# Optimization experiments

Hardware: AMD Instinct MI355X
Metric: run time of the kernel (lower is better)

The kernel has to match this reference:

```python
import jax, jax.numpy as jnp
import numpy as np

EPS = 1e-8  # torch CosineSimilarity eps
TEMP = 0.05

def _l2norm(x):
    n = jnp.sqrt(jnp.sum(x * x, axis=-1, keepdims=True))
    return x / jnp.maximum(n, EPS)

def setup_inputs() -> dict:
    key = jax.random.key(0)
    k1, k2, k3 = jax.random.split(key, 3)
    query = jax.random.normal(k1, (256, 768), dtype=jnp.float32)
    keys = jax.random.normal(k2, (256, 768), dtype=jnp.float32)
    queue = jax.random.normal(k3, (64, 1024, 768), dtype=jnp.float32)
    return {"query": query, "keys": keys, "queue": queue}

def reference(query, keys, queue):
    B, D = query.shape
    qn = _l2norm(query)                       # [B, D]
    kn = _l2norm(keys)                        # [B, D]
    negn = _l2norm(queue.reshape(-1, D))      # [N, D]
    sim_pos = jnp.einsum('bd,cd->bc', qn, kn)   # [B, B]
    sim_neg = jnp.einsum('bd,nd->bn', qn, negn) # [B, N]
    logits = jnp.concatenate([sim_pos, sim_neg], axis=1) / TEMP  # [B, B+N]
    target = jnp.arange(B)
    logp = jax.nn.log_softmax(logits, axis=-1)
    loss = -jnp.mean(logp[jnp.arange(B), target])
    return loss
```

## Files before the change

### kernel.cpp

```cpp
#include <hip/hip_runtime.h>
#include <hip/hip_bf16.h>

typedef __attribute__((ext_vector_type(8))) short short8;
typedef __attribute__((ext_vector_type(4))) float f32x4;

#define TEMP_INV 20.0f
#define NCH 256

__device__ inline unsigned short f2bf(float f){
    unsigned int u = __builtin_bit_cast(unsigned int, f);
    u += 0x7fffu + ((u >> 16) & 1u);
    return (unsigned short)(u >> 16);
}
__device__ inline float bf2f(unsigned short h){
    unsigned int u = ((unsigned int)h) << 16;
    return __builtin_bit_cast(float, u);
}
__device__ inline unsigned int pk2bf(float a, float b){
    return (unsigned int)f2bf(a) | ((unsigned int)f2bf(b) << 16);
}

#define GLOAD16(src, dst) __builtin_amdgcn_global_load_lds( \
    (const __attribute__((address_space(1))) unsigned int*)(src), \
    (__attribute__((address_space(3))) unsigned int*)(dst), 16, 0, 0)

__global__ __launch_bounds__(256) void k_norm(const float* __restrict__ q,
                                              unsigned short* __restrict__ Aswz){
    int b = blockIdx.x, t = threadIdx.x;
    const float* qr = q + b * 768;
    float v0 = qr[t], v1 = qr[t + 256], v2 = qr[t + 512];
    float ss = v0*v0 + v1*v1 + v2*v2;
#pragma unroll
    for (int o = 32; o; o >>= 1) ss += __shfl_xor(ss, o);
    __shared__ float red[4];
    if ((t & 63) == 0) red[t >> 6] = ss;
    __syncthreads();
    ss = red[0] + red[1] + red[2] + red[3];
    float inv = 1.0f / fmaxf(sqrtf(ss), 1e-8f);
    float nv[3] = {v0 * inv, v1 * inv, v2 * inv};
#pragma unroll
    for (int j = 0; j < 3; j++){
        int cc = t + 256 * j;
        unsigned short h = f2bf(nv[j]);
        int kc = cc >> 6, kl = cc & 63, g = kl >> 3, e = kl & 7;
        int slot = g ^ (b & 7);
        Aswz[kc * 16384 + b * 64 + slot * 8 + e] = h;
    }
}

__global__ __launch_bounds__(1024, 1) void k_main(
        const float* __restrict__ keys,
        const float* __restrict__ queue,
        const unsigned short* __restrict__ Aswz,
        float* __restrict__ pmax,
        float* __restrict__ psum,
        float* __restrict__ diag){
    __shared__ unsigned short Atile[2][16384];
    __shared__ unsigned short Btile[8192];
    __shared__ float bxnf[768];
    __shared__ unsigned short bxn16[768];
    __shared__ float invn[128];
    __shared__ float redm[4][256];
    __shared__ float reds[4][256];
    __shared__ float xred[4][256];
    __shared__ float wred[16];
    __shared__ float sxs;

    const int b = blockIdx.x, t = threadIdx.x;
    const int lane = t & 63;
    const int w = t >> 6;
    const int wm = w >> 2, wn = w & 3;
    const int frow = lane & 15, fg = lane >> 4;
    const int c = t >> 3, q8 = t & 7;

    size_t rx = (size_t)b * 257;
    float ssx = 0.f;
    if (t < 768){ float v = queue[rx * 768 + t]; bxnf[t] = v; ssx = v * v; }
#pragma unroll
    for (int o = 32; o; o >>= 1) ssx += __shfl_xor(ssx, o);
    if (lane == 0) wred[w] = ssx;
    __syncthreads();
    if (t == 0){
        float s = 0.f;
#pragma unroll
        for (int i = 0; i < 16; i++) s += wred[i];
        sxs = 1.0f / fmaxf(sqrtf(s), 1e-8f);
    }
    __syncthreads();
    if (t < 768) bxn16[t] = f2bf(bxnf[t] * sxs);
    __syncthreads();

    long n0 = (long)b * 257 + c;
    long n1 = n0 + 128;
    const float* rp0 = ((n0 < 256) ? (keys + n0 * 768)
                                   : (queue + (size_t)(n0 - 256) * 768)) + q8 * 4;
    const float* rp1 = ((n1 < 256) ? (keys + n1 * 768)
                                   : (queue + (size_t)(n1 - 256) * 768)) + q8 * 4;

    {
        const unsigned short* gA = Aswz + t * 8;
        GLOAD16(gA, &Atile[0][t * 8]);
        GLOAD16(gA + 8192, &Atile[0][t * 8 + 8192]);
    }
    float4 cb0 = *(const float4*)(rp0);
    float4 cb1 = *(const float4*)(rp0 + 32);

    float Mrun = -1e30f, Srun = 0.f;
    float dx = 0.f;
    const int xrow = t & 255, xk = t >> 8;

    for (int p = 0; p < 2; ++p){
        const float* rp = p ? rp1 : rp0;
        float ssq = 0.f;
        f32x4 acc[4][2];
#pragma unroll
        for (int i = 0; i < 4; i++)
#pragma unroll
            for (int j = 0; j < 2; j++) acc[i][j] = (f32x4)0.f;

        for (int kc = 0; kc < 12; ++kc){
            const int s = p * 12 + kc;
            const bool lastStep = (s == 23);
            float4 nb0 = cb0, nb1 = cb1;
            if (!lastStep){
                const int sn = s + 1;
                const int kcn = (kc < 11) ? (kc + 1) : 0;
                const unsigned short* gA = Aswz + kcn * 16384 + t * 8;
                unsigned short* lA = &Atile[sn & 1][t * 8];
                GLOAD16(gA, lA);
                GLOAD16(gA + 8192, lA + 8192);
                const float* rpn = (kc < 11) ? rp : rp1;
                nb0 = *(const float4*)(rpn + kcn * 64);
                nb1 = *(const float4*)(rpn + kcn * 64 + 32);
                asm volatile("s_waitcnt vmcnt(4)" ::: "memory");
            } else {
                asm volatile("s_waitcnt vmcnt(0)" ::: "memory");
            }

            {
                float4 u = cb0;
                ssq += u.x*u.x + u.y*u.y + u.z*u.z + u.w*u.w;
                int idx = q8;
                int slot = (idx >> 1) ^ (c & 7);
                uint2 pk;
                pk.x = pk2bf(u.x, u.y);
                pk.y = pk2bf(u.z, u.w);
                *(uint2*)&Btile[c * 64 + slot * 8 + (idx & 1) * 4] = pk;
                u = cb1;
                ssq += u.x*u.x + u.y*u.y + u.z*u.z + u.w*u.w;
                idx = q8 + 8;
                slot = (idx >> 1) ^ (c & 7);
                pk.x = pk2bf(u.x, u.y);
                pk.y = pk2bf(u.z, u.w);
                *(uint2*)&Btile[c * 64 + slot * 8 + (idx & 1) * 4] = pk;
            }
            asm volatile("s_waitcnt lgkmcnt(0)" ::: "memory");
            __builtin_amdgcn_s_barrier();
            asm volatile("" ::: "memory");

#pragma unroll
            for (int ks = 0; ks < 2; ++ks){
                short8 af[4], bfv[2];
#pragma unroll
                for (int fm = 0; fm < 4; ++fm){
                    int row = wm * 64 + fm * 16 + frow;
                    int slot = (ks * 4 + fg) ^ (frow & 7);
                    af[fm] = *(const short8*)&Atile[s & 1][row * 64 + slot * 8];
                }
#pragma unroll
                for (int fn = 0; fn < 2; ++fn){
                    int row = wn * 32 + fn * 16 + frow;
                    int slot = (ks * 4 + fg) ^ (frow & 7);
                    bfv[fn] = *(const short8*)&Btile[row * 64 + slot * 8];
                }
#pragma unroll
                for (int fm = 0; fm < 4; ++fm)
#pragma unroll
                    for (int fn = 0; fn < 2; ++fn)
                        acc[fm][fn] = __builtin_amdgcn_mfma_f32_16x16x32_bf16(
                            af[fm], bfv[fn], acc[fm][fn], 0, 0, 0);
            }

            if (p == 0){
#pragma unroll
                for (int gi = 0; gi < 2; ++gi){
                    int g = xk * 2 + gi;
                    short8 av = *(const short8*)&Atile[kc & 1][xrow * 64 + (g ^ (xrow & 7)) * 8];
                    short8 xv = *(const short8*)&bxn16[kc * 64 + g * 8];
#pragma unroll
                    for (int e = 0; e < 8; ++e)
                        dx += bf2f((unsigned short)av[e]) * bf2f((unsigned short)xv[e]);
                }
            }

            __builtin_amdgcn_s_barrier();
            asm volatile("" ::: "memory");
            cb0 = nb0; cb1 = nb1;
        }

        ssq += __shfl_xor(ssq, 1);
        ssq += __shfl_xor(ssq, 2);
        ssq += __shfl_xor(ssq, 4);
        if (q8 == 0) invn[c] = 1.0f / fmaxf(sqrtf(ssq), 1e-8f);
        if (p == 0) xred[xk][xrow] = dx;
        __syncthreads();

#pragma unroll
        for (int fm = 0; fm < 4; ++fm){
#pragma unroll
            for (int rr = 0; rr < 4; ++rr){
                float v0 = acc[fm][0][rr] * invn[wn * 32 + frow] * TEMP_INV;
                float v1 = acc[fm][1][rr] * invn[wn * 32 + 16 + frow] * TEMP_INV;
                int row = wm * 64 + fm * 16 + fg * 4 + rr;
                if (b == 0){
                    int col0 = p * 128 + wn * 32 + frow;
                    if (row == col0)      diag[row] = v0;
                    if (row == col0 + 16) diag[row] = v1;
                }
                float m = fmaxf(v0, v1);
#pragma unroll
                for (int o = 1; o < 16; o <<= 1) m = fmaxf(m, __shfl_xor(m, o));
                float s = __expf(v0 - m) + __expf(v1 - m);
#pragma unroll
                for (int o = 1; o < 16; o <<= 1) s += __shfl_xor(s, o);
                if (frow == 0){ redm[wn][row] = m; reds[wn][row] = s; }
            }
        }
        __syncthreads();
        if (t < 256){
#pragma unroll
            for (int ww = 0; ww < 4; ++ww){
                float m2 = redm[ww][t], s2 = reds[ww][t];
                float M = fmaxf(Mrun, m2);
                Srun = Srun * __expf(Mrun - M) + s2 * __expf(m2 - M);
                Mrun = M;
            }
        }
        __syncthreads();
    }

    if (t < 256){
        float vx = (xred[0][t] + xred[1][t] + xred[2][t] + xred[3][t]) * TEMP_INV;
        float M = fmaxf(Mrun, vx);
        float S = Srun * __expf(Mrun - M) + __expf(vx - M);
        pmax[b * 256 + t] = M;
        psum[b * 256 + t] = S;
    }
}

__global__ __launch_bounds__(256) void k_lse(const float* __restrict__ pmax,
                                             const float* __restrict__ psum,
                                             const float* __restrict__ diag,
                                             float* __restrict__ lossb){
    int b = blockIdx.x, t = threadIdx.x;
    float m = -1e30f;
    for (int cc = t; cc < NCH; cc += 256) m = fmaxf(m, pmax[cc * 256 + b]);
#pragma unroll
    for (int o = 32; o; o >>= 1) m = fmaxf(m, __shfl_xor(m, o));
    __shared__ float red[4];
    __shared__ float Msh;
    if ((t & 63) == 0) red[t >> 6] = m;
    __syncthreads();
    if (t == 0) Msh = fmaxf(fmaxf(red[0], red[1]), fmaxf(red[2], red[3]));
    __syncthreads();
    float M = Msh;
    float s = 0.f;
    for (int cc = t; cc < NCH; cc += 256) s += psum[cc * 256 + b] * __expf(pmax[cc * 256 + b] - M);
#pragma unroll
    for (int o = 32; o; o >>= 1) s += __shfl_xor(s, o);
    if ((t & 63) == 0) red[t >> 6] = s;
    __syncthreads();
    if (t == 0) lossb[b] = M + logf(red[0] + red[1] + red[2] + red[3]) - diag[b];
}

__global__ __launch_bounds__(256) void k_red(const float* __restrict__ lossb,
                                             float* __restrict__ out){
    int t = threadIdx.x;
    float v = lossb[t];
#pragma unroll
    for (int o = 32; o; o >>= 1) v += __shfl_xor(v, o);
    __shared__ float red[4];
    if ((t & 63) == 0) red[t >> 6] = v;
    __syncthreads();
    if (t == 0) out[0] = (red[0] + red[1] + red[2] + red[3]) * (1.0f / 256.0f);
}

extern "C" void kernel_launch(void* const* d_in, const int* in_sizes, int n_in,
                              void* d_out, int out_size, void* d_ws, size_t ws_size,
                              hipStream_t stream){
    const float* q  = (const float*)d_in[0];
    const float* k  = (const float*)d_in[1];
    const float* qu = (const float*)d_in[2];
    char* ws = (char*)d_ws;
    unsigned short* Aswz = (unsigned short*)(ws);
    float* diag  = (float*)(ws + 393216);
    float* pmax  = (float*)(ws + 394240);
    float* psum  = (float*)(ws + 656384);
    float* lossb = (float*)(ws + 918528);

    k_norm<<<256, 256, 0, stream>>>(q, Aswz);
    k_main<<<256, 1024, 0, stream>>>(k, qu, Aswz, pmax, psum, diag);
    k_lse<<<256, 256, 0, stream>>>(pmax, psum, diag, lossb);
    k_red<<<1, 256, 0, stream>>>(lossb, (float*)d_out);
}
```

Measured before the change: 71.24 us.

## Double-buffer B tile, flatten k-loop, and fuse final reduction via atomicAdd

Double-buffers the B tile in LDS and prefetches B rows two steps ahead, so staging the next B chunk overlaps the current MFMA step and one barrier per iteration goes away. The two passes are flattened into a single 24-step loop, with the first pass's softmax epilogue placed at step 11. The separate final reduction kernel is removed: k_lse atomically adds each row's scaled loss into the output, which k_norm now zeroes. This saves a kernel launch and some barrier stalls, at the cost of extra LDS and a float atomic sum whose ordering is nondeterministic.

```diff
diff --git a/kernel.cpp b/kernel.cpp
--- a/kernel.cpp
+++ b/kernel.cpp
@@ -25,8 +25,10 @@
     (__attribute__((address_space(3))) unsigned int*)(dst), 16, 0, 0)
 
 __global__ __launch_bounds__(256) void k_norm(const float* __restrict__ q,
-                                              unsigned short* __restrict__ Aswz){
+                                              unsigned short* __restrict__ Aswz,
+                                              float* __restrict__ out){
     int b = blockIdx.x, t = threadIdx.x;
+    if (b == 0 && t == 0) out[0] = 0.f;
     const float* qr = q + b * 768;
     float v0 = qr[t], v1 = qr[t + 256], v2 = qr[t + 512];
     float ss = v0*v0 + v1*v1 + v2*v2;
@@ -56,7 +58,7 @@
         float* __restrict__ psum,
         float* __restrict__ diag){
     __shared__ unsigned short Atile[2][16384];
-    __shared__ unsigned short Btile[8192];
+    __shared__ unsigned short Btile[2][8192];
     __shared__ float bxnf[768];
     __shared__ unsigned short bxn16[768];
     __shared__ float invn[128];
@@ -72,6 +74,7 @@
     const int wm = w >> 2, wn = w & 3;
     const int frow = lane & 15, fg = lane >> 4;
     const int c = t >> 3, q8 = t & 7;
+    const int c7 = c & 7;
 
     size_t rx = (size_t)b * 257;
     float ssx = 0.f;
@@ -97,114 +100,168 @@
     const float* rp1 = ((n1 < 256) ? (keys + n1 * 768)
                                    : (queue + (size_t)(n1 - 256) * 768)) + q8 * 4;
 
+    float ssqA = 0.f, ssqB = 0.f;
+
+    auto stageB = [&](unsigned short* bt, float4 u0, float4 u1, float& sq){
+        sq += u0.x*u0.x + u0.y*u0.y + u0.z*u0.z + u0.w*u0.w;
+        sq += u1.x*u1.x + u1.y*u1.y + u1.z*u1.z + u1.w*u1.w;
+        int slot0 = (q8 >> 1) ^ c7;
+        int slot1 = ((q8 + 8) >> 1) ^ c7;
+        uint2 pk0, pk1;
+        pk0.x = pk2bf(u0.x, u0.y); pk0.y = pk2bf(u0.z, u0.w);
+        pk1.x = pk2bf(u1.x, u1.y); pk1.y = pk2bf(u1.z, u1.w);
+        *(uint2*)&bt[c * 64 + slot0 * 8 + (q8 & 1) * 4] = pk0;
+        *(uint2*)&bt[c * 64 + slot1 * 8 + (q8 & 1) * 4] = pk1;
+    };
+
     {
         const unsigned short* gA = Aswz + t * 8;
         GLOAD16(gA, &Atile[0][t * 8]);
         GLOAD16(gA + 8192, &Atile[0][t * 8 + 8192]);
     }
-    float4 cb0 = *(const float4*)(rp0);
-    float4 cb1 = *(const float4*)(rp0 + 32);
+    float4 cur0 = *(const float4*)(rp0);
+    float4 cur1 = *(const float4*)(rp0 + 32);
+    float4 nxt0 = *(const float4*)(rp0 + 64);
+    float4 nxt1 = *(const float4*)(rp0 + 96);
+    asm volatile("s_waitcnt vmcnt(2)" ::: "memory");
+    stageB(Btile[0], cur0, cur1, ssqA);
+    asm volatile("s_waitcnt lgkmcnt(0)" ::: "memory");
+    __builtin_amdgcn_s_barrier();
+    asm volatile("" ::: "memory");
+    cur0 = nxt0; cur1 = nxt1;
 
     float Mrun = -1e30f, Srun = 0.f;
     float dx = 0.f;
     const int xrow = t & 255, xk = t >> 8;
 
-    for (int p = 0; p < 2; ++p){
-        const float* rp = p ? rp1 : rp0;
-        float ssq = 0.f;
-        f32x4 acc[4][2];
-#pragma unroll
-        for (int i = 0; i < 4; i++)
-#pragma unroll
-            for (int j = 0; j < 2; j++) acc[i][j] = (f32x4)0.f;
-
-        for (int kc = 0; kc < 12; ++kc){
-            const int s = p * 12 + kc;
-            const bool lastStep = (s == 23);
-            float4 nb0 = cb0, nb1 = cb1;
-            if (!lastStep){
-                const int sn = s + 1;
-                const int kcn = (kc < 11) ? (kc + 1) : 0;
-                const unsigned short* gA = Aswz + kcn * 16384 + t * 8;
-                unsigned short* lA = &Atile[sn & 1][t * 8];
-                GLOAD16(gA, lA);
-                GLOAD16(gA + 8192, lA + 8192);
-                const float* rpn = (kc < 11) ? rp : rp1;
-                nb0 = *(const float4*)(rpn + kcn * 64);
-                nb1 = *(const float4*)(rpn + kcn * 64 + 32);
-                asm volatile("s_waitcnt vmcnt(4)" ::: "memory");
-            } else {
-                asm volatile("s_waitcnt vmcnt(0)" ::: "memory");
-            }
-
-            {
-                float4 u = cb0;
-                ssq += u.x*u.x + u.y*u.y + u.z*u.z + u.w*u.w;
-                int idx = q8;
-                int slot = (idx >> 1) ^ (c & 7);
-                uint2 pk;
-                pk.x = pk2bf(u.x, u.y);
-                pk.y = pk2bf(u.z, u.w);
-                *(uint2*)&Btile[c * 64 + slot * 8 + (idx & 1) * 4] = pk;
-                u = cb1;
-                ssq += u.x*u.x + u.y*u.y + u.z*u.z + u.w*u.w;
-                idx = q8 + 8;
-                slot = (idx >> 1) ^ (c & 7);
-                pk.x = pk2bf(u.x, u.y);
-                pk.y = pk2bf(u.z, u.w);
-                *(uint2*)&Btile[c * 64 + slot * 8 + (idx & 1) * 4] = pk;
-            }
-            asm volatile("s_waitcnt lgkmcnt(0)" ::: "memory");
-            __builtin_amdgcn_s_barrier();
-            asm volatile("" ::: "memory");
-
-#pragma unroll
-            for (int ks = 0; ks < 2; ++ks){
-                short8 af[4], bfv[2];
-#pragma unroll
-                for (int fm = 0; fm < 4; ++fm){
-                    int row = wm * 64 + fm * 16 + frow;
-                    int slot = (ks * 4 + fg) ^ (frow & 7);
-                    af[fm] = *(const short8*)&Atile[s & 1][row * 64 + slot * 8];
+    f32x4 acc[4][2];
+#pragma unroll
+    for (int i = 0; i < 4; i++)
+#pragma unroll
+        for (int j = 0; j < 2; j++) acc[i][j] = (f32x4)0.f;
+
+    for (int s = 0; s < 24; ++s){
+        if (s < 23){
+            int kcn = (s + 1) % 12;
+            const unsigned short* gA = Aswz + kcn * 16384 + t * 8;
+            unsigned short* lA = &Atile[(s + 1) & 1][t * 8];
+            GLOAD16(gA, lA);
+            GLOAD16(gA + 8192, lA + 8192);
+        }
+        float4 nb0 = cur0, nb1 = cur1;
+        if (s < 22){
+            int u = s + 2;
+            const float* rpu = (u < 12) ? rp0 : rp1;
+            int kcu = (u < 12) ? u : (u - 12);
+            nb0 = *(const float4*)(rpu + kcu * 64);
+            nb1 = *(const float4*)(rpu + kcu * 64 + 32);
+        }
+        if (s < 22)       asm volatile("s_waitcnt vmcnt(4)" ::: "memory");
+        else if (s == 22) asm volatile("s_waitcnt vmcnt(2)" ::: "memory");
+        else              asm volatile("s_waitcnt vmcnt(0)" ::: "memory");
+
+        if (s < 23){
+            int u = s + 1;
+            if (u < 12) stageB(Btile[(s + 1) & 1], cur0, cur1, ssqA);
+            else        stageB(Btile[(s + 1) & 1], cur0, cur1, ssqB);
+        }
+
+        const unsigned short* At = Atile[s & 1];
+        const unsigned short* Bt = Btile[s & 1];
+#pragma unroll
+        for (int ks = 0; ks < 2; ++ks){
+            short8 af[4], bfv[2];
+#pragma unroll
+            for (int fm = 0; fm < 4; ++fm){
+                int row = wm * 64 + fm * 16 + frow;
+                int slot = (ks * 4 + fg) ^ (frow & 7);
+                af[fm] = *(const short8*)&At[row * 64 + slot * 8];
+            }
+#pragma unroll
+            for (int fn = 0; fn < 2; ++fn){
+                int row = wn * 32 + fn * 16 + frow;
+                int slot = (ks * 4 + fg) ^ (frow & 7);
+                bfv[fn] = *(const short8*)&Bt[row * 64 + slot * 8];
+            }
+#pragma unroll
+            for (int fm = 0; fm < 4; ++fm)
+#pragma unroll
+                for (int fn = 0; fn < 2; ++fn)
+                    acc[fm][fn] = __builtin_amdgcn_mfma_f32_16x16x32_bf16(
+                        af[fm], bfv[fn], acc[fm][fn], 0, 0, 0);
+        }
+
+        if (s < 12){
+#pragma unroll
+            for (int gi = 0; gi < 2; ++gi){
+                int g = xk * 2 + gi;
+                short8 av = *(const short8*)&At[xrow * 64 + (g ^ (xrow & 7)) * 8];
+                short8 xv = *(const short8*)&bxn16[s * 64 + g * 8];
+#pragma unroll
+                for (int e = 0; e < 8; ++e)
+                    dx += bf2f((unsigned short)av[e]) * bf2f((unsigned short)xv[e]);
+            }
+        }
+
+        asm volatile("s_waitcnt lgkmcnt(0)" ::: "memory");
+        __builtin_amdgcn_s_barrier();
+        asm volatile("" ::: "memory");
+        cur0 = nb0; cur1 = nb1;
+
+        if (s == 11){
+            float sq = ssqA;
+            sq += __shfl_xor(sq, 1);
+            sq += __shfl_xor(sq, 2);
+            sq += __shfl_xor(sq, 4);
+            if (q8 == 0) invn[c] = 1.0f / fmaxf(sqrtf(sq), 1e-8f);
+            xred[xk][xrow] = dx;
+            __syncthreads();
+#pragma unroll
+            for (int fm = 0; fm < 4; ++fm){
+#pragma unroll
+                for (int rr = 0; rr < 4; ++rr){
+                    float v0 = acc[fm][0][rr] * invn[wn * 32 + frow] * TEMP_INV;
+                    float v1 = acc[fm][1][rr] * invn[wn * 32 + 16 + frow] * TEMP_INV;
+                    int row = wm * 64 + fm * 16 + fg * 4 + rr;
+                    if (b == 0){
+                        int col0 = wn * 32 + frow;
+                        if (row == col0)      diag[row] = v0;
+                        if (row == col0 + 16) diag[row] = v1;
+                    }
+                    float m = fmaxf(v0, v1);
+#pragma unroll
+                    for (int o = 1; o < 16; o <<= 1) m = fmaxf(m, __shfl_xor(m, o));
+                    float sex = __expf(v0 - m) + __expf(v1 - m);
+#pragma unroll
+                    for (int o = 1; o < 16; o <<= 1) sex += __shfl_xor(sex, o);
+                    if (frow == 0){ redm[wn][row] = m; reds[wn][row] = sex; }
                 }
-#pragma unroll
-                for (int fn = 0; fn < 2; ++fn){
-                    int row = wn * 32 + fn * 16 + frow;
-                    int slot = (ks * 4 + fg) ^ (frow & 7);
-                    bfv[fn] = *(const short8*)&Btile[row * 64 + slot * 8];
+            }
+            __syncthreads();
+            if (t < 256){
+#pragma unroll
+                for (int ww = 0; ww < 4; ++ww){
+                    float m2 = redm[ww][t], s2 = reds[ww][t];
+                    float M = fmaxf(Mrun, m2);
+                    Srun = Srun * __expf(Mrun - M) + s2 * __expf(m2 - M);
+                    Mrun = M;
                 }
-#pragma unroll
-                for (int fm = 0; fm < 4; ++fm)
-#pragma unroll
-                    for (int fn = 0; fn < 2; ++fn)
-                        acc[fm][fn] = __builtin_amdgcn_mfma_f32_16x16x32_bf16(
-                            af[fm], bfv[fn], acc[fm][fn], 0, 0, 0);
-            }
-
-            if (p == 0){
-#pragma unroll
-                for (int gi = 0; gi < 2; ++gi){
-                    int g = xk * 2 + gi;
-                    short8 av = *(const short8*)&Atile[kc & 1][xrow * 64 + (g ^ (xrow & 7)) * 8];
-                    short8 xv = *(const short8*)&bxn16[kc * 64 + g * 8];
-#pragma unroll
-                    for (int e = 0; e < 8; ++e)
-                        dx += bf2f((unsigned short)av[e]) * bf2f((unsigned short)xv[e]);
-                }
-            }
-
-            __builtin_amdgcn_s_barrier();
-            asm volatile("" ::: "memory");
-            cb0 = nb0; cb1 = nb1;
-        }
-
-        ssq += __shfl_xor(ssq, 1);
-        ssq += __shfl_xor(ssq, 2);
-        ssq += __shfl_xor(ssq, 4);
-        if (q8 == 0) invn[c] = 1.0f / fmaxf(sqrtf(ssq), 1e-8f);
-        if (p == 0) xred[xk][xrow] = dx;
+            }
+            __syncthreads();
+#pragma unroll
+            for (int i = 0; i < 4; i++)
+#pragma unroll
+                for (int j = 0; j < 2; j++) acc[i][j] = (f32x4)0.f;
+        }
+    }
+
+    {
+        float sq = ssqB;
+        sq += __shfl_xor(sq, 1);
+        sq += __shfl_xor(sq, 2);
+        sq += __shfl_xor(sq, 4);
+        if (q8 == 0) invn[c] = 1.0f / fmaxf(sqrtf(sq), 1e-8f);
         __syncthreads();
-
 #pragma unroll
         for (int fm = 0; fm < 4; ++fm){
 #pragma unroll
@@ -213,17 +270,17 @@
                 float v1 = acc[fm][1][rr] * invn[wn * 32 + 16 + frow] * TEMP_INV;
                 int row = wm * 64 + fm * 16 + fg * 4 + rr;
                 if (b == 0){
-                    int col0 = p * 128 + wn * 32 + frow;
+                    int col0 = 128 + wn * 32 + frow;
                     if (row == col0)      diag[row] = v0;
                     if (row == col0 + 16) diag[row] = v1;
                 }
                 float m = fmaxf(v0, v1);
 #pragma unroll
                 for (int o = 1; o < 16; o <<= 1) m = fmaxf(m, __shfl_xor(m, o));
-                float s = __expf(v0 - m) + __expf(v1 - m);
-#pragma unroll
-                for (int o = 1; o < 16; o <<= 1) s += __shfl_xor(s, o);
-                if (frow == 0){ redm[wn][row] = m; reds[wn][row] = s; }
+                float sex = __expf(v0 - m) + __expf(v1 - m);
+#pragma unroll
+                for (int o = 1; o < 16; o <<= 1) sex += __shfl_xor(sex, o);
+                if (frow == 0){ redm[wn][row] = m; reds[wn][row] = sex; }
             }
         }
         __syncthreads();
@@ -236,7 +293,6 @@
                 Mrun = M;
             }
         }
-        __syncthreads();
     }
 
     if (t < 256){
@@ -251,7 +307,7 @@
 __global__ __launch_bounds__(256) void k_lse(const float* __restrict__ pmax,
                                              const float* __restrict__ psum,
                                              const float* __restrict__ diag,
-                                             float* __restrict__ lossb){
+                                             float* __restrict__ out){
     int b = blockIdx.x, t = threadIdx.x;
     float m = -1e30f;
     for (int cc = t; cc < NCH; cc += 256) m = fmaxf(m, pmax[cc * 256 + b]);
@@ -270,19 +326,8 @@
     for (int o = 32; o; o >>= 1) s += __shfl_xor(s, o);
     if ((t & 63) == 0) red[t >> 6] = s;
     __syncthreads();
-    if (t == 0) lossb[b] = M + logf(red[0] + red[1] + red[2] + red[3]) - diag[b];
-}
-
-__global__ __launch_bounds__(256) void k_red(const float* __restrict__ lossb,
-                                             float* __restrict__ out){
-    int t = threadIdx.x;
-    float v = lossb[t];
-#pragma unroll
-    for (int o = 32; o; o >>= 1) v += __shfl_xor(v, o);
-    __shared__ float red[4];
-    if ((t & 63) == 0) red[t >> 6] = v;
-    __syncthreads();
-    if (t == 0) out[0] = (red[0] + red[1] + red[2] + red[3]) * (1.0f / 256.0f);
+    if (t == 0)
+        atomicAdd(out, (M + logf(red[0] + red[1] + red[2] + red[3]) - diag[b]) * (1.0f / 256.0f));
 }
 
 extern "C" void kernel_launch(void* const* d_in, const int* in_sizes, int n_in,
@@ -296,10 +341,8 @@
     float* diag  = (float*)(ws + 393216);
     float* pmax  = (float*)(ws + 394240);
     float* psum  = (float*)(ws + 656384);
-    float* lossb = (float*)(ws + 918528);
-
-    k_norm<<<256, 256, 0, stream>>>(q, Aswz);
+
+    k_norm<<<256, 256, 0, stream>>>(q, Aswz, (float*)d_out);
     k_main<<<256, 1024, 0, stream>>>(k, qu, Aswz, pmax, psum, diag);
-    k_lse<<<256, 256, 0, stream>>>(pmax, psum, diag, lossb);
-    k_red<<<1, 256, 0, stream>>>(lossb, (float*)d_out);
-}
+    k_lse<<<256, 256, 0, stream>>>(pmax, psum, diag, (float*)d_out);
+}
```

Measured after the change: 71.31 us. Within noise of the previous version (+0.1%).

## Split main GEMM into 1024 smaller blocks and fuse final reduction via atomics

Applied to the files above, without the earlier changes.

The main kernel now runs 1024 blocks of 512 threads, each handling 64 queue rows, instead of 256 blocks of 1024 threads handling 257 rows. Keys are handled only as a single-row diagonal dot product in the first 256 blocks, since only the diagonal of the positive block is used. The explicit double-buffered A prefetch with manual waitcnt is replaced by a simple load-sync-compute loop that relies on multiple resident blocks per CU for latency hiding. The final reduction kernel is dropped in favour of an atomicAdd into the zeroed output, which introduces a nondeterministic summation order.

```diff
diff --git a/kernel.cpp b/kernel.cpp
--- a/kernel.cpp
+++ b/kernel.cpp
@@ -5,7 +5,7 @@
 typedef __attribute__((ext_vector_type(4))) float f32x4;
 
 #define TEMP_INV 20.0f
-#define NCH 256
+#define NCH 1024
 
 __device__ inline unsigned short f2bf(float f){
     unsigned int u = __builtin_bit_cast(unsigned int, f);
@@ -25,8 +25,10 @@
     (__attribute__((address_space(3))) unsigned int*)(dst), 16, 0, 0)
 
 __global__ __launch_bounds__(256) void k_norm(const float* __restrict__ q,
-                                              unsigned short* __restrict__ Aswz){
+                                              unsigned short* __restrict__ Aswz,
+                                              float* __restrict__ out){
     int b = blockIdx.x, t = threadIdx.x;
+    if (b == 0 && t == 0) out[0] = 0.f;
     const float* qr = q + b * 768;
     float v0 = qr[t], v1 = qr[t + 256], v2 = qr[t + 512];
     float ss = v0*v0 + v1*v1 + v2*v2;
@@ -48,201 +50,154 @@
     }
 }
 
-__global__ __launch_bounds__(1024, 1) void k_main(
+__global__ __launch_bounds__(512, 4) void k_main(
         const float* __restrict__ keys,
         const float* __restrict__ queue,
         const unsigned short* __restrict__ Aswz,
         float* __restrict__ pmax,
         float* __restrict__ psum,
         float* __restrict__ diag){
-    __shared__ unsigned short Atile[2][16384];
-    __shared__ unsigned short Btile[8192];
-    __shared__ float bxnf[768];
+    __shared__ unsigned short Atile[16384];
+    __shared__ unsigned short Btile[4096];
     __shared__ unsigned short bxn16[768];
-    __shared__ float invn[128];
-    __shared__ float redm[4][256];
-    __shared__ float reds[4][256];
-    __shared__ float xred[4][256];
-    __shared__ float wred[16];
+    __shared__ float invn[64];
+    __shared__ float redm[2][256];
+    __shared__ float reds[2][256];
+    __shared__ float xred[2][256];
+    __shared__ float wred[8];
     __shared__ float sxs;
 
     const int b = blockIdx.x, t = threadIdx.x;
     const int lane = t & 63;
     const int w = t >> 6;
-    const int wm = w >> 2, wn = w & 3;
+    const int wm = w >> 1, wn = w & 1;
     const int frow = lane & 15, fg = lane >> 4;
-    const int c = t >> 3, q8 = t & 7;
-
-    size_t rx = (size_t)b * 257;
-    float ssx = 0.f;
-    if (t < 768){ float v = queue[rx * 768 + t]; bxnf[t] = v; ssx = v * v; }
-#pragma unroll
-    for (int o = 32; o; o >>= 1) ssx += __shfl_xor(ssx, o);
-    if (lane == 0) wred[w] = ssx;
-    __syncthreads();
-    if (t == 0){
-        float s = 0.f;
-#pragma unroll
-        for (int i = 0; i < 16; i++) s += wred[i];
-        sxs = 1.0f / fmaxf(sqrtf(s), 1e-8f);
-    }
-    __syncthreads();
-    if (t < 768) bxn16[t] = f2bf(bxnf[t] * sxs);
-    __syncthreads();
-
-    long n0 = (long)b * 257 + c;
-    long n1 = n0 + 128;
-    const float* rp0 = ((n0 < 256) ? (keys + n0 * 768)
-                                   : (queue + (size_t)(n0 - 256) * 768)) + q8 * 4;
-    const float* rp1 = ((n1 < 256) ? (keys + n1 * 768)
-                                   : (queue + (size_t)(n1 - 256) * 768)) + q8 * 4;
-
-    {
-        const unsigned short* gA = Aswz + t * 8;
-        GLOAD16(gA, &Atile[0][t * 8]);
-        GLOAD16(gA + 8192, &Atile[0][t * 8 + 8192]);
-    }
-    float4 cb0 = *(const float4*)(rp0);
-    float4 cb1 = *(const float4*)(rp0 + 32);
-
-    float Mrun = -1e30f, Srun = 0.f;
-    float dx = 0.f;
+    const int r = t >> 3, q8 = t & 7;
+    const bool keyblk = (b < 256);
+
+    if (keyblk){
+        const float* krow = keys + b * 768;
+        float v0 = krow[t];
+        float v1 = (t < 256) ? krow[512 + t] : 0.f;
+        float ssx = v0 * v0 + v1 * v1;
+#pragma unroll
+        for (int o = 32; o; o >>= 1) ssx += __shfl_xor(ssx, o);
+        if (lane == 0) wred[w] = ssx;
+        __syncthreads();
+        if (t == 0){
+            float s = 0.f;
+#pragma unroll
+            for (int i = 0; i < 8; i++) s += wred[i];
+            sxs = 1.0f / fmaxf(sqrtf(s), 1e-8f);
+        }
+        __syncthreads();
+        bxn16[t] = f2bf(v0 * sxs);
+        if (t < 256) bxn16[512 + t] = f2bf(v1 * sxs);
+        __syncthreads();
+    }
+
+    const float* rp = queue + (size_t)(b * 64 + r) * 768 + q8 * 4;
     const int xrow = t & 255, xk = t >> 8;
 
-    for (int p = 0; p < 2; ++p){
-        const float* rp = p ? rp1 : rp0;
-        float ssq = 0.f;
-        f32x4 acc[4][2];
+    float ssq = 0.f, dx = 0.f;
+    f32x4 acc[4][2];
+#pragma unroll
+    for (int i = 0; i < 4; i++)
+#pragma unroll
+        for (int j = 0; j < 2; j++) acc[i][j] = (f32x4)0.f;
+
+    for (int kc = 0; kc < 12; ++kc){
+        if (kc) __syncthreads();
 #pragma unroll
         for (int i = 0; i < 4; i++)
-#pragma unroll
-            for (int j = 0; j < 2; j++) acc[i][j] = (f32x4)0.f;
-
-        for (int kc = 0; kc < 12; ++kc){
-            const int s = p * 12 + kc;
-            const bool lastStep = (s == 23);
-            float4 nb0 = cb0, nb1 = cb1;
-            if (!lastStep){
-                const int sn = s + 1;
-                const int kcn = (kc < 11) ? (kc + 1) : 0;
-                const unsigned short* gA = Aswz + kcn * 16384 + t * 8;
-                unsigned short* lA = &Atile[sn & 1][t * 8];
-                GLOAD16(gA, lA);
-                GLOAD16(gA + 8192, lA + 8192);
-                const float* rpn = (kc < 11) ? rp : rp1;
-                nb0 = *(const float4*)(rpn + kcn * 64);
-                nb1 = *(const float4*)(rpn + kcn * 64 + 32);
-                asm volatile("s_waitcnt vmcnt(4)" ::: "memory");
-            } else {
-                asm volatile("s_waitcnt vmcnt(0)" ::: "memory");
+            GLOAD16(Aswz + kc * 16384 + i * 4096 + t * 8,
+                    Atile + i * 4096 + t * 8);
+        float4 u0 = *(const float4*)(rp + kc * 64);
+        float4 u1 = *(const float4*)(rp + kc * 64 + 32);
+        ssq += u0.x*u0.x + u0.y*u0.y + u0.z*u0.z + u0.w*u0.w;
+        ssq += u1.x*u1.x + u1.y*u1.y + u1.z*u1.z + u1.w*u1.w;
+        {
+            int slot0 = (q8 >> 1) ^ (r & 7);
+            int slot1 = ((q8 + 8) >> 1) ^ (r & 7);
+            uint2 pk0, pk1;
+            pk0.x = pk2bf(u0.x, u0.y); pk0.y = pk2bf(u0.z, u0.w);
+            pk1.x = pk2bf(u1.x, u1.y); pk1.y = pk2bf(u1.z, u1.w);
+            *(uint2*)&Btile[r * 64 + slot0 * 8 + (q8 & 1) * 4] = pk0;
+            *(uint2*)&Btile[r * 64 + slot1 * 8 + (q8 & 1) * 4] = pk1;
+        }
+        __syncthreads();
+
+#pragma unroll
+        for (int ks = 0; ks < 2; ++ks){
+            short8 af[4], bfv[2];
+#pragma unroll
+            for (int fm = 0; fm < 4; ++fm){
+                int row = wm * 64 + fm * 16 + frow;
+                int slot = (ks * 4 + fg) ^ (frow & 7);
+                af[fm] = *(const short8*)&Atile[row * 64 + slot * 8];
             }
-
-            {
-                float4 u = cb0;
-                ssq += u.x*u.x + u.y*u.y + u.z*u.z + u.w*u.w;
-                int idx = q8;
-                int slot = (idx >> 1) ^ (c & 7);
-                uint2 pk;
-                pk.x = pk2bf(u.x, u.y);
-                pk.y = pk2bf(u.z, u.w);
-                *(uint2*)&Btile[c * 64 + slot * 8 + (idx & 1) * 4] = pk;
-                u = cb1;
-                ssq += u.x*u.x + u.y*u.y + u.z*u.z + u.w*u.w;
-                idx = q8 + 8;
-                slot = (idx >> 1) ^ (c & 7);
-                pk.x = pk2bf(u.x, u.y);
-                pk.y = pk2bf(u.z, u.w);
-                *(uint2*)&Btile[c * 64 + slot * 8 + (idx & 1) * 4] = pk;
+#pragma unroll
+            for (int fn = 0; fn < 2; ++fn){
+                int row = wn * 32 + fn * 16 + frow;
+                int slot = (ks * 4 + fg) ^ (frow & 7);
+                bfv[fn] = *(const short8*)&Btile[row * 64 + slot * 8];
             }
-            asm volatile("s_waitcnt lgkmcnt(0)" ::: "memory");
-            __builtin_amdgcn_s_barrier();
-            asm volatile("" ::: "memory");
-
-#pragma unroll
-            for (int ks = 0; ks < 2; ++ks){
-                short8 af[4], bfv[2];
-#pragma unroll
-                for (int fm = 0; fm < 4; ++fm){
-                    int row = wm * 64 + fm * 16 + frow;
-                    int slot = (ks * 4 + fg) ^ (frow & 7);
-                    af[fm] = *(const short8*)&Atile[s & 1][row * 64 + slot * 8];
-                }
-#pragma unroll
-                for (int fn = 0; fn < 2; ++fn){
-                    int row = wn * 32 + fn * 16 + frow;
-                    int slot = (ks * 4 + fg) ^ (frow & 7);
-                    bfv[fn] = *(const short8*)&Btile[row * 64 + slot * 8];
-                }
-#pragma unroll
-                for (int fm = 0; fm < 4; ++fm)
-#pragma unroll
-                    for (int fn = 0; fn < 2; ++fn)
-                        acc[fm][fn] = __builtin_amdgcn_mfma_f32_16x16x32_bf16(
-                            af[fm], bfv[fn], acc[fm][fn], 0, 0, 0);
+#pragma unroll
+            for (int fm = 0; fm < 4; ++fm)
+#pragma unroll
+                for (int fn = 0; fn < 2; ++fn)
+                    acc[fm][fn] = __builtin_amdgcn_mfma_f32_16x16x32_bf16(
+                        af[fm], bfv[fn], acc[fm][fn], 0, 0, 0);
+        }
+
+        if (keyblk){
+#pragma unroll
+            for (int gi = 0; gi < 4; ++gi){
+                int g = xk * 4 + gi;
+                short8 av = *(const short8*)&Atile[xrow * 64 + (g ^ (xrow & 7)) * 8];
+                short8 xv = *(const short8*)&bxn16[kc * 64 + g * 8];
+#pragma unroll
+                for (int e = 0; e < 8; ++e)
+                    dx += bf2f((unsigned short)av[e]) * bf2f((unsigned short)xv[e]);
             }
-
-            if (p == 0){
-#pragma unroll
-                for (int gi = 0; gi < 2; ++gi){
-                    int g = xk * 2 + gi;
-                    short8 av = *(const short8*)&Atile[kc & 1][xrow * 64 + (g ^ (xrow & 7)) * 8];
-                    short8 xv = *(const short8*)&bxn16[kc * 64 + g * 8];
-#pragma unroll
-                    for (int e = 0; e < 8; ++e)
-                        dx += bf2f((unsigned short)av[e]) * bf2f((unsigned short)xv[e]);
-                }
-            }
-
-            __builtin_amdgcn_s_barrier();
-            asm volatile("" ::: "memory");
-            cb0 = nb0; cb1 = nb1;
-        }
-
-        ssq += __shfl_xor(ssq, 1);
-        ssq += __shfl_xor(ssq, 2);
-        ssq += __shfl_xor(ssq, 4);
-        if (q8 == 0) invn[c] = 1.0f / fmaxf(sqrtf(ssq), 1e-8f);
-        if (p == 0) xred[xk][xrow] = dx;
-        __syncthreads();
-
-#pragma unroll
-        for (int fm = 0; fm < 4; ++fm){
-#pragma unroll
-            for (int rr = 0; rr < 4; ++rr){
-                float v0 = acc[fm][0][rr] * invn[wn * 32 + frow] * TEMP_INV;
-                float v1 = acc[fm][1][rr] * invn[wn * 32 + 16 + frow] * TEMP_INV;
-                int row = wm * 64 + fm * 16 + fg * 4 + rr;
-                if (b == 0){
-                    int col0 = p * 128 + wn * 32 + frow;
-                    if (row == col0)      diag[row] = v0;
-                    if (row == col0 + 16) diag[row] = v1;
-                }
-                float m = fmaxf(v0, v1);
-#pragma unroll
-                for (int o = 1; o < 16; o <<= 1) m = fmaxf(m, __shfl_xor(m, o));
-                float s = __expf(v0 - m) + __expf(v1 - m);
-#pragma unroll
-                for (int o = 1; o < 16; o <<= 1) s += __shfl_xor(s, o);
-                if (frow == 0){ redm[wn][row] = m; reds[wn][row] = s; }
-            }
-        }
-        __syncthreads();
-        if (t < 256){
-#pragma unroll
-            for (int ww = 0; ww < 4; ++ww){
-                float m2 = redm[ww][t], s2 = reds[ww][t];
-                float M = fmaxf(Mrun, m2);
-                Srun = Srun * __expf(Mrun - M) + s2 * __expf(m2 - M);
-                Mrun = M;
-            }
-        }
-        __syncthreads();
-    }
-
+        }
+    }
+
+    ssq += __shfl_xor(ssq, 1);
+    ssq += __shfl_xor(ssq, 2);
+    ssq += __shfl_xor(ssq, 4);
+    if (q8 == 0) invn[r] = 1.0f / fmaxf(sqrtf(ssq), 1e-8f);
+    if (keyblk) xred[xk][xrow] = dx;
+    __syncthreads();
+
+#pragma unroll
+    for (int fm = 0; fm < 4; ++fm){
+#pragma unroll
+        for (int rr = 0; rr < 4; ++rr){
+            float v0 = acc[fm][0][rr] * invn[wn * 32 + frow] * TEMP_INV;
+            float v1 = acc[fm][1][rr] * invn[wn * 32 + 16 + frow] * TEMP_INV;
+            int row = wm * 64 + fm * 16 + fg * 4 + rr;
+            float m = fmaxf(v0, v1);
+#pragma unroll
+            for (int o = 1; o < 16; o <<= 1) m = fmaxf(m, __shfl_xor(m, o));
+            float s = __expf(v0 - m) + __expf(v1 - m);
+#pragma unroll
+            for (int o = 1; o < 16; o <<= 1) s += __shfl_xor(s, o);
+            if (frow == 0){ redm[wn][row] = m; reds[wn][row] = s; }
+        }
+    }
+    __syncthreads();
     if (t < 256){
-        float vx = (xred[0][t] + xred[1][t] + xred[2][t] + xred[3][t]) * TEMP_INV;
-        float M = fmaxf(Mrun, vx);
-        float S = Srun * __expf(Mrun - M) + __expf(vx - M);
+        float m0 = redm[0][t], m1 = redm[1][t];
+        float M = fmaxf(m0, m1);
+        float S = reds[0][t] * __expf(m0 - M) + reds[1][t] * __expf(m1 - M);
+        if (keyblk){
+            float vx = (xred[0][t] + xred[1][t]) * TEMP_INV;
+            if (t == b) diag[b] = vx;
+            float M2 = fmaxf(M, vx);
+            S = S * __expf(M - M2) + __expf(vx - M2);
+            M = M2;
+        }
         pmax[b * 256 + t] = M;
         psum[b * 256 + t] = S;
     }
@@ -251,7 +206,7 @@
 __global__ __launch_bounds__(256) void k_lse(const float* __restrict__ pmax,
                                              const float* __restrict__ psum,
                                              const float* __restrict__ diag,
-                                             float* __restrict__ lossb){
+                                             float* __restrict__ out){
     int b = blockIdx.x, t = threadIdx.x;
     float m = -1e30f;
     for (int cc = t; cc < NCH; cc += 256) m = fmaxf(m, pmax[cc * 256 + b]);
@@ -270,19 +225,8 @@
     for (int o = 32; o; o >>= 1) s += __shfl_xor(s, o);
     if ((t & 63) == 0) red[t >> 6] = s;
     __syncthreads();
-    if (t == 0) lossb[b] = M + logf(red[0] + red[1] + red[2] + red[3]) - diag[b];
-}
-
-__global__ __launch_bounds__(256) void k_red(const float* __restrict__ lossb,
-                                             float* __restrict__ out){
-    int t = threadIdx.x;
-    float v = lossb[t];
-#pragma unroll
-    for (int o = 32; o; o >>= 1) v += __shfl_xor(v, o);
-    __shared__ float red[4];
-    if ((t & 63) == 0) red[t >> 6] = v;
-    __syncthreads();
-    if (t == 0) out[0] = (red[0] + red[1] + red[2] + red[3]) * (1.0f / 256.0f);
+    if (t == 0)
+        atomicAdd(out, (M + logf(red[0] + red[1] + red[2] + red[3]) - diag[b]) * (1.0f / 256.0f));
 }
 
 extern "C" void kernel_launch(void* const* d_in, const int* in_sizes, int n_in,
@@ -295,11 +239,9 @@
     unsigned short* Aswz = (unsigned short*)(ws);
     float* diag  = (float*)(ws + 393216);
     float* pmax  = (float*)(ws + 394240);
-    float* psum  = (float*)(ws + 656384);
-    float* lossb = (float*)(ws + 918528);
-
-    k_norm<<<256, 256, 0, stream>>>(q, Aswz);
-    k_main<<<256, 1024, 0, stream>>>(k, qu, Aswz, pmax, psum, diag);
-    k_lse<<<256, 256, 0, stream>>>(pmax, psum, diag, lossb);
-    k_red<<<1, 256, 0, stream>>>(lossb, (float*)d_out);
-}
+    float* psum  = (float*)(ws + 1442816);
+
+    k_norm<<<256, 256, 0, stream>>>(q, Aswz, (float*)d_out);
+    k_main<<<1024, 512, 0, stream>>>(k, qu, Aswz, pmax, psum, diag);
+    k_lse<<<256, 256, 0, stream>>>(pmax, psum, diag, (float*)d_out);
+}
```

Result: slower. 78.49 us (+10.2%).
